# Optimization experiments

Measured on AMD Instinct MI355X. Metric: run time of the kernel, lower is better.

The kernel has to match this reference:

```python
import jax, jax.numpy as jnp
import numpy as np

B = 1
DIM = 128
NUM_HEADS = 8
HEAD_DIM = DIM // NUM_HEADS
RES = (4, 16, 16, 16)            # (L, D, H, W)
FINE = (2, 8, 8, 8)
COARSE = (1, 2, 2, 2)
FINE_STRIDE = tuple(r // f for r, f in zip(RES, FINE))      # (2,2,2,2)
COARSE_STRIDE = tuple(r // c for r, c in zip(RES, COARSE))  # (4,8,8,8)
LOCAL = (1, 2, 2, 2)
HIDDEN = 512
SCALE = HEAD_DIM ** -0.5
EPS = 1e-5
_DN = jax.lax.ConvDimensionNumbers((0, 1, 2, 3, 4, 5), (0, 1, 2, 3, 4, 5), (0, 1, 2, 3, 4, 5))


def conv4d(x, w, b, stride=(1, 1, 1, 1)):
    # x: (B, L, C, D, H, W); channel axis is 2 (matches repo Conv4d usage). 'same'-style k//2 pad.
    xc = jnp.transpose(x, (0, 2, 1, 3, 4, 5))  # B,C,L,D,H,W
    pads = [(k // 2, k // 2) for k in w.shape[2:]]
    y = jax.lax.conv_general_dilated(xc, w, window_strides=stride, padding=pads, dimension_numbers=_DN)
    y = y + b[None, :, None, None, None, None]
    return jnp.transpose(y, (0, 2, 1, 3, 4, 5))


def layernorm(x, w, b):
    mu = jnp.mean(x, -1, keepdims=True)
    var = jnp.mean(jnp.square(x - mu), -1, keepdims=True)
    return (x - mu) * jax.lax.rsqrt(var + EPS) * w + b


def cnorm(x, w, b):
    # LayerNorm over channel axis (axis 2) of (B,L,C,D,H,W)
    xt = jnp.transpose(x, (0, 1, 3, 4, 5, 2))
    xt = layernorm(xt, w, b)
    return jnp.transpose(xt, (0, 1, 5, 2, 3, 4))


def to_tokens(t):
    # (B,L,C,D,H,W) -> (B, L*D*H*W, C)
    b, c = t.shape[0], t.shape[2]
    return jnp.swapaxes(jnp.transpose(t, (0, 2, 1, 3, 4, 5)).reshape(b, c, -1), 1, 2)


def split_heads(t):
    b, n, c = t.shape
    return jnp.transpose(t.reshape(b, n, NUM_HEADS, c // NUM_HEADS), (0, 2, 1, 3))


def slg(x, q_w, q_b, k_w, k_b, v_w, v_b, p_w, p_b, f_w, f_b, c_w, c_b, ln_w, ln_b):
    Bx, L, C, D, H, W = x.shape
    N = L * D * H * W
    q = split_heads(to_tokens(conv4d(x, q_w, q_b)))          # (B,h,N,hd)
    xc = conv4d(x, c_w, c_b, COARSE_STRIDE)                  # coarse pyramid (B,1,C,2,2,2)
    xf = conv4d(x, f_w, f_b, FINE_STRIDE)                    # fine pyramid   (B,2,C,8,8,8)
    kc = to_tokens(conv4d(xc, k_w, k_b))
    kf = to_tokens(conv4d(xf, k_w, k_b))
    vc = to_tokens(conv4d(xc, v_w, v_b))
    vf = to_tokens(conv4d(xf, v_w, v_b))
    k = split_heads(layernorm(jnp.concatenate([kc, kf], 1), ln_w, ln_b))
    v = split_heads(layernorm(jnp.concatenate([vc, vf], 1), ln_w, ln_b))
    attn = jax.nn.softmax(jnp.einsum('bhqd,bhkd->bhqk', q, k) * SCALE, axis=-1)
    y = jnp.einsum('bhqk,bhkd->bhqd', attn, v)               # (B,h,N,hd)
    y = jnp.transpose(y, (0, 2, 1, 3)).reshape(Bx, N, C)
    y = jnp.swapaxes(jnp.swapaxes(y, 1, 2).reshape(Bx, C, L, D, H, W), 1, 2)
    return conv4d(y, p_w, p_b)


def _win(t):
    # (B,Lh,C,D,H,W) -> (B, n_windows, heads, win_tokens, hd)
    b, l, c, d, h, w = t.shape
    ll, ld, lh, lw = LOCAL
    nl, nd, nh, nw = l // ll, d // ld, h // lh, w // lw
    t = jnp.transpose(t, (0, 2, 1, 3, 4, 5)).reshape(b, c, nl, ll, nd, ld, nh, lh, nw, lw)
    t = jnp.transpose(t, (0, 2, 4, 6, 8, 3, 5, 7, 9, 1))
    t = t.reshape(b, nl * nd * nh * nw, ll * ld * lh * lw, NUM_HEADS, c // NUM_HEADS)
    return jnp.transpose(t, (0, 1, 3, 2, 4))


def _unwin(y, shape):
    b, l, c, d, h, w = shape
    ll, ld, lh, lw = LOCAL
    nl, nd, nh, nw = l // ll, d // ld, h // lh, w // lw
    y = jnp.transpose(y, (0, 1, 3, 2, 4)).reshape(b, nl, nd, nh, nw, ll, ld, lh, lw, c)
    y = jnp.transpose(y, (0, 9, 1, 5, 2, 6, 3, 7, 4, 8)).reshape(b, c, l, d, h, w)
    return jnp.swapaxes(y, 1, 2)


def tlg(x, q_w, q_b, k_w, k_b, v_w, v_b, p_w, p_b):
    # stage < 2: first temporal half cross-attends with second half (windowed)
    L = x.shape[1]
    xs, xe = x[:, :L // 2], x[:, L // 2:]

    def cross(xq, xkv):
        q = _win(conv4d(xq, q_w, q_b))
        k = _win(conv4d(xkv, k_w, k_b))
        v = _win(conv4d(xkv, v_w, v_b))
        a = jax.nn.softmax(jnp.einsum('bnhqd,bnhkd->bnhqk', q, k) * SCALE, axis=-1)
        y = _unwin(jnp.einsum('bnhqk,bnhkd->bnhqd', a, v), xq.shape)
        return conv4d(y, p_w, p_b)

    return jnp.concatenate([cross(xs, xe), cross(xe, xs)], axis=1)


def _forward(x, n1_w, n1_b, tq_w, tq_b, tk_w, tk_b, tv_w, tv_b, tp_w, tp_b,
             n2_w, n2_b, sq_w, sq_b, sk_w, sk_b, sv_w, sv_b, sp_w, sp_b,
             sf_w, sf_b, sc_w, sc_b, sn_w, sn_b,
             n3_w, n3_b, m1_w, m1_b, m2_w, m2_b):
    x = x + tlg(cnorm(x, n1_w, n1_b), tq_w, tq_b, tk_w, tk_b, tv_w, tv_b, tp_w, tp_b)
    x = x + slg(cnorm(x, n2_w, n2_b), sq_w, sq_b, sk_w, sk_b, sv_w, sv_b, sp_w, sp_b,
                sf_w, sf_b, sc_w, sc_b, sn_w, sn_b)
    x = x + conv4d(jax.nn.relu(conv4d(cnorm(x, n3_w, n3_b), m1_w, m1_b)), m2_w, m2_b)
    return x


def setup_inputs():
    keys = iter(jax.random.split(jax.random.key(0), 64))

    def rn(shape, s=0.02):
        return jax.random.normal(next(keys), shape, dtype=jnp.float32) * s

    L, D, H, W = RES
    inp = {"x": jax.random.normal(next(keys), (B, L, DIM, D, H, W), dtype=jnp.float32)}
    for n in ("n1", "n2", "n3", "sn"):
        inp[n + "_w"] = jnp.ones((DIM,), jnp.float32)
        inp[n + "_b"] = jnp.zeros((DIM,), jnp.float32)
    for n in ("tq", "tk", "tv", "tp"):
        inp[n + "_w"] = rn((DIM, DIM, 3, 1, 1, 1))
        inp[n + "_b"] = jnp.zeros((DIM,), jnp.float32)
    for n in ("sq", "sk", "sv", "sp", "sf", "sc"):
        inp[n + "_w"] = rn((DIM, DIM, 1, 3, 3, 3))
        inp[n + "_b"] = jnp.zeros((DIM,), jnp.float32)
    inp["m1_w"] = rn((HIDDEN, DIM, 3, 3, 3, 3))
    inp["m1_b"] = jnp.zeros((HIDDEN,), jnp.float32)
    inp["m2_w"] = rn((DIM, HIDDEN, 3, 3, 3, 3))
    inp["m2_b"] = jnp.zeros((DIM,), jnp.float32)
    return inp


def reference(x, n1_w, n1_b, n2_w, n2_b, n3_w, n3_b, sn_w, sn_b,
              tq_w, tq_b, tk_w, tk_b, tv_w, tv_b, tp_w, tp_b,
              sq_w, sq_b, sk_w, sk_b, sv_w, sv_b, sp_w, sp_b,
              sf_w, sf_b, sc_w, sc_b, m1_w, m1_b, m2_w, m2_b):
    return _forward(x, n1_w, n1_b, tq_w, tq_b, tk_w, tk_b, tv_w, tv_b, tp_w, tp_b,
                    n2_w, n2_b, sq_w, sq_b, sk_w, sk_b, sv_w, sv_b, sp_w, sp_b,
                    sf_w, sf_b, sc_w, sc_b, sn_w, sn_b,
                    n3_w, n3_b, m1_w, m1_b, m2_w, m2_b)
```

## Files before the change

### kernel.cpp

```cpp
#include <hip/hip_runtime.h>

typedef unsigned short u16;
typedef __attribute__((ext_vector_type(8))) short bf16x8;
typedef __attribute__((ext_vector_type(4))) float f32x4;

#define PITCH 40

__device__ __forceinline__ u16 f2bf(float f) {
  union { float f; unsigned u; } v; v.f = f;
  unsigned r = v.u + 0x7fffu + ((v.u >> 16) & 1u);
  return (u16)(r >> 16);
}
__device__ __forceinline__ float bf2f(u16 h) {
  union { unsigned u; float f; } v; v.u = ((unsigned)h) << 16;
  return v.f;
}
__device__ __forceinline__ float4 load4bf(const u16* p) {
  ushort4 h = *(const ushort4*)p;
  return make_float4(bf2f(h.x), bf2f(h.y), bf2f(h.z), bf2f(h.w));
}
__device__ __forceinline__ void gll16(const u16* g, u16* l) {
  __builtin_amdgcn_global_load_lds(
      (const __attribute__((address_space(1))) unsigned int*)g,
      (__attribute__((address_space(3))) unsigned int*)l, 16, 0, 0);
}

__device__ __forceinline__ ushort2 ln_row(float2 v, float2 gv, float2 bv) {
  float s = v.x + v.y;
#pragma unroll
  for (int o = 32; o > 0; o >>= 1) s += __shfl_xor(s, o);
  float mu = s * (1.0f / 128.0f);
  float dx = v.x - mu, dy = v.y - mu;
  float q = dx * dx + dy * dy;
#pragma unroll
  for (int o = 32; o > 0; o >>= 1) q += __shfl_xor(q, o);
  float rs = rsqrtf(q * (1.0f / 128.0f) + 1e-5f);
  ushort2 o2;
  o2.x = f2bf(dx * rs * gv.x + bv.x);
  o2.y = f2bf(dy * rs * gv.y + bv.y);
  return o2;
}

__global__ __launch_bounds__(256) void k_tin_ln(const float* __restrict__ x,
                                                float* __restrict__ X0,
                                                const float* __restrict__ g,
                                                const float* __restrict__ b,
                                                u16* __restrict__ XN) {
  __shared__ float t[128][33];
  int s0 = blockIdx.x * 32, l = blockIdx.y;
  int tid = threadIdx.x;
#pragma unroll
  for (int r = 0; r < 4; ++r) {
    int lin = r * 256 + tid;
    int c = lin >> 3, sq = (lin & 7) * 4;
    float4 v = *(const float4*)(x + ((long)(l * 128 + c) << 12) + s0 + sq);
    t[c][sq] = v.x; t[c][sq + 1] = v.y; t[c][sq + 2] = v.z; t[c][sq + 3] = v.w;
  }
  __syncthreads();
  int wave = tid >> 6, lane = tid & 63;
  int c2 = lane * 2;
  float2 gv = *(const float2*)(g + c2);
  float2 bv = *(const float2*)(b + c2);
#pragma unroll
  for (int p = 0; p < 8; ++p) {
    int s = p * 4 + wave;
    float2 v = make_float2(t[c2][s], t[c2 + 1][s]);
    long token = (long)l * 4096 + s0 + s;
    *(float2*)(X0 + token * 128 + c2) = v;
    ushort2 o2 = ln_row(v, gv, bv);
    *(ushort2*)(XN + token * 128 + c2) = o2;
  }
}

struct RAargs { const float* w[12]; u16* wb[12]; u16* zp; };
__global__ __launch_bounds__(256) void k_repack_all(RAargs a) {
  __shared__ float ws[128 * 81];
  int z = blockIdx.z, x = blockIdx.x, tid = threadIdx.x;
  if (z == 0 && x == 0) ((unsigned long long*)a.zp)[tid] = 0ull;
  if (z < 10 && x >= 128) return;
  int NT = (z < 4) ? 3 : ((z < 10) ? 27 : 81);
  int OC = (z == 10) ? 512 : 128;
  int IC = (z == 11) ? 512 : 128;
  int oc, ic0;
  if (z == 11) { oc = x & 127; ic0 = (x >> 7) << 7; }
  else { oc = x; ic0 = 0; }
  const float* src = a.w[z] + ((long)oc * IC + ic0) * NT;
  int n = 128 * NT;
  for (int i = tid; i < n; i += 256) ws[i] = src[i];
  __syncthreads();
  u16* dst = a.wb[z] + (long)oc * IC + ic0;
  long tstep = (long)OC * IC;
  for (int idx = tid; idx < n; idx += 256) {
    int t = idx >> 7, i = idx & 127;
    dst[(long)t * tstep + i] = f2bf(ws[i * NT + t]);
  }
}

struct QC {
  const u16* X[4]; const u16* W[4]; const float* B[4]; void* Y[4];
  int M[4];
  int lgo[4][3];
  int lgi[4][3];
  int di[4][3];
  int st[4][4];
  int flags[4];
};
__global__ __launch_bounds__(256) void k_conv_quad(QC a) {
  __shared__ u16 As[64 * PITCH];
  __shared__ u16 Bs[64 * PITCH];
  int grp = blockIdx.z;
  int M = a.M[grp];
  int m0 = blockIdx.x * 64;
  if (m0 >= M) return;
  const u16* X = a.X[grp];
  const u16* W3 = a.W[grp];
  const float* bias = a.B[grp];
  void* Yv = a.Y[grp];
  int lgWo = a.lgo[grp][0], lgHo = a.lgo[grp][1], lgDo = a.lgo[grp][2];
  int lgWi = a.lgi[grp][0], lgHi = a.lgi[grp][1], lgDi = a.lgi[grp][2];
  int Di = a.di[grp][0], Hi = a.di[grp][1], Wi = a.di[grp][2];
  int sL = a.st[grp][0], sD = a.st[grp][1], sH = a.st[grp][2], sW = a.st[grp][3];
  int flags = a.flags[grp];

  int tid = threadIdx.x;
  int wave = tid >> 6, lane = tid & 63;
  int quad = lane >> 4, l15 = lane & 15;
  int oc0 = blockIdx.y * 64;

  int srl = tid >> 2;
  int sao = (tid & 3) * 8;
  int sboc = tid >> 2, sbo = (tid & 3) * 8;

  int sm = m0 + srl;
  bool mv = sm < M;
  int w = sm & ((1 << lgWo) - 1);
  int h = (sm >> lgWo) & ((1 << lgHo) - 1);
  int d = (sm >> (lgWo + lgHo)) & ((1 << lgDo) - 1);
  int l = sm >> (lgWo + lgHo + lgDo);

  int c0 = 0, c1 = 0, c2 = 0, c3 = 0;
  auto comp_nb = [&]() -> long {
    if (!mv) return -1;
    int li = l * sL, di = d * sD + c2 - 1, hi = h * sH + c1 - 1, wi = w * sW + c0 - 1;
    bool ok = ((unsigned)di < (unsigned)Di) && ((unsigned)hi < (unsigned)Hi) &&
              ((unsigned)wi < (unsigned)Wi);
    (void)c3;
    if (!ok) return -1;
    return ((((long)((li << lgDi) + di) << lgHi) + hi) << lgWi) + wi;
  };

  long nb = comp_nb();
  const u16* wt = W3 + (long)(oc0 + sboc) * 128 + sbo;
  const long wstep = 128 * 128;
  const int kmask = 3;
  const int total = 27 * 4;

  const bf16x8 Z = {0, 0, 0, 0, 0, 0, 0, 0};
  bf16x8 ra0 = Z, rb;
  if (nb >= 0) ra0 = *(const bf16x8*)(X + nb * 128 + sao);
  rb = *(const bf16x8*)wt;

  f32x4 acc[4];
#pragma unroll
  for (int j = 0; j < 4; ++j) acc[j] = {0.f, 0.f, 0.f, 0.f};

  int wrow = wave * 16;

  for (int ks = 0; ks < total; ++ks) {
    __syncthreads();
    *(bf16x8*)&As[srl * PITCH + sao] = ra0;
    *(bf16x8*)&Bs[sboc * PITCH + sbo] = rb;
    __syncthreads();
    int ksn = ks + 1;
    if (ksn < total) {
      int k0n = (ksn & kmask) << 5;
      if ((ksn & kmask) == 0) {
        wt += wstep;
        if (++c0 == 3) { c0 = 0; if (++c1 == 3) { c1 = 0; if (++c2 == 3) { c2 = 0; ++c3; } } }
        nb = comp_nb();
      }
      ra0 = Z;
      if (nb >= 0) ra0 = *(const bf16x8*)(X + nb * 128 + k0n + sao);
      rb = *(const bf16x8*)(wt + k0n);
    }
    bf16x8 a0 = *(const bf16x8*)&As[(wrow + l15) * PITCH + quad * 8];
#pragma unroll
    for (int j = 0; j < 4; ++j) {
      bf16x8 b = *(const bf16x8*)&Bs[(j * 16 + l15) * PITCH + quad * 8];
      acc[j] = __builtin_amdgcn_mfma_f32_16x16x32_bf16(a0, b, acc[j], 0, 0, 0);
    }
  }

  int col = oc0 + l15;
#pragma unroll
  for (int j = 0; j < 4; ++j) {
    float bj = bias[col + j * 16];
    int rbase = m0 + wrow + quad * 4;
#pragma unroll
    for (int r = 0; r < 4; ++r) {
      int row = rbase + r;
      if (row >= M) continue;
      float v = acc[j][r] + bj;
      if (flags & 2) v = fmaxf(v, 0.f);
      long off = (long)row * 128 + col + j * 16;
      if (flags & 4) ((u16*)Yv)[off] = f2bf(v);
      else if (flags & 1) ((float*)Yv)[off] += v;
      else ((float*)Yv)[off] = v;
    }
  }
}

__global__ __launch_bounds__(256, 4) void k_conv_gl(
    const u16* __restrict__ X, const u16* __restrict__ W3,
    const float* __restrict__ bias, void* __restrict__ Yv, float* __restrict__ SP,
    const u16* __restrict__ ZP,
    int M, int IC, int OC, int mode, int NT, int NSPLIT, long wgs,
    int lgWo, int lgHo, int lgDo,
    int lgWi, int lgHi, int lgDi,
    int Li, int Di, int Hi, int Wi,
    int sL, int sD, int sH, int sW, int flags) {
  __shared__ __align__(16) u16 As[128 * 64];
  __shared__ __align__(16) u16 Bs[128 * 64];
  int tid = threadIdx.x;
  int wave = tid >> 6, lane = tid & 63;
  int quad = lane >> 4, l15 = lane & 15;
  int m0 = blockIdx.x * 128, oc0 = blockIdx.y * 128;
  int mi = wave & 1, ni = wave >> 1;
  int zz = blockIdx.z;
  int grp = zz / NSPLIT, split = zz % NSPLIT;
  W3 += (long)grp * wgs;

  int rp[4], cA[4], sm[4];
#pragma unroll
  for (int q = 0; q < 4; ++q) {
    rp[q] = wave * 32 + q * 8 + (lane >> 3);
    cA[q] = ((lane & 7) - (rp[q] >> 1)) & 7;
    sm[q] = m0 + rp[q];
  }

  int tap_per = (NT + NSPLIT - 1) / NSPLIT;
  int t0 = split * tap_per;
  int t1 = min(NT, t0 + tap_per);
  int kc = IC >> 6;
  int total = (t1 - t0) * kc;

  int c0 = t0 % 3, c1 = (t0 / 3) % 3, c2 = (t0 / 9) % 3, c3 = t0 / 27;
  auto comp_nb = [&](int smv) -> int {
    if (smv >= M) return -1;
    int w = smv & ((1 << lgWo) - 1);
    int h = (smv >> lgWo) & ((1 << lgHo) - 1);
    int d = (smv >> (lgWo + lgHo)) & ((1 << lgDo) - 1);
    int l = smv >> (lgWo + lgHo + lgDo);
    int li, di, hi, wi; bool ok;
    if (mode == 0) {
      int dl = c0 - 1;
      int ll = (l & 1) + dl;
      ok = (ll >= 0 && ll < 2);
      li = l + dl; di = d; hi = h; wi = w;
    } else if (mode == 1) {
      li = l * sL; di = d * sD + c2 - 1; hi = h * sH + c1 - 1; wi = w * sW + c0 - 1;
      ok = ((unsigned)di < (unsigned)Di) && ((unsigned)hi < (unsigned)Hi) &&
           ((unsigned)wi < (unsigned)Wi);
    } else {
      li = l + c3 - 1; di = d + c2 - 1; hi = h + c1 - 1; wi = w + c0 - 1;
      ok = ((unsigned)li < (unsigned)Li) && ((unsigned)di < (unsigned)Di) &&
           ((unsigned)hi < (unsigned)Hi) && ((unsigned)wi < (unsigned)Wi);
    }
    if (!ok) return -1;
    return (((li << lgDi) + di) << lgHi | hi) << lgWi | wi;
  };

  int nb[4];
#pragma unroll
  for (int q = 0; q < 4; ++q) nb[q] = comp_nb(sm[q]);
  long wstep = (long)OC * IC;
  const u16* wbase = W3 + (long)t0 * wstep + (long)oc0 * IC;

  f32x4 acc[4][4];
#pragma unroll
  for (int i = 0; i < 4; ++i)
#pragma unroll
    for (int j = 0; j < 4; ++j) acc[i][j] = {0.f, 0.f, 0.f, 0.f};

  int kk = 0;
  for (int ks = 0; ks < total; ++ks) {
    if (kk == kc) {
      kk = 0;
      if (++c0 == 3) { c0 = 0; if (++c1 == 3) { c1 = 0; if (++c2 == 3) { c2 = 0; ++c3; } } }
#pragma unroll
      for (int q = 0; q < 4; ++q) nb[q] = comp_nb(sm[q]);
      wbase += wstep;
    }
    int k0 = kk << 6;
    ++kk;
    __syncthreads();
#pragma unroll
    for (int q = 0; q < 4; ++q) {
      const u16* a = (nb[q] >= 0) ? X + (long)nb[q] * IC + k0 + cA[q] * 8 : ZP;
      gll16(a, &As[(wave * 4 + q) * 512]);
    }
#pragma unroll
    for (int q = 0; q < 4; ++q) {
      const u16* bsrc = wbase + (long)rp[q] * IC + k0 + cA[q] * 8;
      gll16(bsrc, &Bs[(wave * 4 + q) * 512]);
    }
    __syncthreads();
#pragma unroll
    for (int ksub = 0; ksub < 2; ++ksub) {
      bf16x8 af[4], bf[4];
#pragma unroll
      for (int i = 0; i < 4; ++i) {
        int row = mi * 64 + i * 16 + l15;
        int pa = ((ksub * 4 + quad) + (row >> 1)) & 7;
        af[i] = *(const bf16x8*)&As[row * 64 + pa * 8];
      }
#pragma unroll
      for (int j = 0; j < 4; ++j) {
        int row = ni * 64 + j * 16 + l15;
        int pb = ((ksub * 4 + quad) + (row >> 1)) & 7;
        bf[j] = *(const bf16x8*)&Bs[row * 64 + pb * 8];
      }
#pragma unroll
      for (int i = 0; i < 4; ++i)
#pragma unroll
        for (int j = 0; j < 4; ++j)
          acc[i][j] = __builtin_amdgcn_mfma_f32_16x16x32_bf16(af[i], bf[j], acc[i][j], 0, 0, 0);
    }
  }

  if (NSPLIT > 1) {
    float* out = SP + (long)(grp * NSPLIT + split) * M * OC;
#pragma unroll
    for (int j = 0; j < 4; ++j) {
      int c = oc0 + ni * 64 + j * 16 + l15;
#pragma unroll
      for (int i = 0; i < 4; ++i) {
        int rbase = m0 + mi * 64 + i * 16 + quad * 4;
#pragma unroll
        for (int r = 0; r < 4; ++r) {
          int row = rbase + r;
          if (row < M) out[(long)row * OC + c] = acc[i][j][r];
        }
      }
    }
  } else {
#pragma unroll
    for (int j = 0; j < 4; ++j) {
      int c = oc0 + ni * 64 + j * 16 + l15;
      float bj = bias[c];
#pragma unroll
      for (int i = 0; i < 4; ++i) {
        int rbase = m0 + mi * 64 + i * 16 + quad * 4;
#pragma unroll
        for (int r = 0; r < 4; ++r) {
          int row = rbase + r;
          if (row >= M) continue;
          float v = acc[i][j][r] + bj;
          if (flags & 2) v = fmaxf(v, 0.f);
          long off = (long)row * OC + c;
          if (flags & 4) ((u16*)Yv)[off] = f2bf(v);
          else if (flags & 1) ((float*)Yv)[off] += v;
          else ((float*)Yv)[off] = v;
        }
      }
    }
  }
}

__global__ __launch_bounds__(512, 2) void k_conv_g256(
    const u16* __restrict__ X, const u16* __restrict__ W3,
    const float* __restrict__ bias, void* __restrict__ Yv, float* __restrict__ SP,
    const u16* __restrict__ ZP,
    int M, int IC, int OC, int mode, int NT, int NSPLIT,
    int lgWo, int lgHo, int lgDo,
    int lgWi, int lgHi, int lgDi,
    int Li, int Di, int Hi, int Wi,
    int sL, int sD, int sH, int sW, int flags) {
  __shared__ __align__(16) u16 Ab[4][8192];
  __shared__ __align__(16) u16 Bb[4][8192];
  int tid = threadIdx.x;
  int wave = tid >> 6, lane = tid & 63;
  int quad = lane >> 4, l15 = lane & 15;
  int wr = wave >> 2, wc = wave & 3;
  int m0 = blockIdx.x * 256, oc0 = blockIdx.y * 256;

  int srow0 = tid >> 2;
  int spc = tid & 3;
  int lc0 = (spc - (srow0 >> 1)) & 3;
  int lc1 = (spc - ((srow0 + 128) >> 1)) & 3;

  int kc = IC >> 6;
  int hsPerTap = kc << 1;
  int tap_per = (NT + NSPLIT - 1) / NSPLIT;
  int t0 = blockIdx.z * tap_per;
  int t1 = min(NT, t0 + tap_per);
  int TOT = (t1 - t0) * kc;
  int TOTH = TOT * 2;

  int c0 = t0 % 3, c1 = (t0 / 3) % 3, c2 = (t0 / 9) % 3, c3 = t0 / 27;
  auto comp_nb = [&](int smv) -> int {
    if (smv >= M) return -1;
    int w = smv & ((1 << lgWo) - 1);
    int h = (smv >> lgWo) & ((1 << lgHo) - 1);
    int d = (smv >> (lgWo + lgHo)) & ((1 << lgDo) - 1);
    int l = smv >> (lgWo + lgHo + lgDo);
    int li, di, hi, wi; bool ok;
    if (mode == 0) {
      int dl = c0 - 1;
      int ll = (l & 1) + dl;
      ok = (ll >= 0 && ll < 2);
      li = l + dl; di = d; hi = h; wi = w;
    } else if (mode == 1) {
      li = l * sL; di = d * sD + c2 - 1; hi = h * sH + c1 - 1; wi = w * sW + c0 - 1;
      ok = ((unsigned)di < (unsigned)Di) && ((unsigned)hi < (unsigned)Hi) &&
           ((unsigned)wi < (unsigned)Wi);
    } else {
      li = l + c3 - 1; di = d + c2 - 1; hi = h + c1 - 1; wi = w + c0 - 1;
      ok = ((unsigned)li < (unsigned)Li) && ((unsigned)di < (unsigned)Di) &&
// ... 126 lines not shown
  }

  if (NSPLIT > 1) {
    float* outp = SP + (long)blockIdx.z * M * OC;
#pragma unroll
    for (int i = 0; i < 8; ++i)
#pragma unroll
      for (int j = 0; j < 4; ++j) {
        int c = oc0 + (wc << 6) + (j << 4) + l15;
        int rb = m0 + (wr << 7) + (i << 4) + (quad << 2);
#pragma unroll
        for (int r = 0; r < 4; ++r) {
          int row = rb + r;
          if (row < M) outp[(long)row * OC + c] = acc[i][j][r];
        }
      }
  } else {
#pragma unroll
    for (int i = 0; i < 8; ++i)
#pragma unroll
      for (int j = 0; j < 4; ++j) {
        int c = oc0 + (wc << 6) + (j << 4) + l15;
        float bj = bias[c];
        int rb = m0 + (wr << 7) + (i << 4) + (quad << 2);
#pragma unroll
        for (int r = 0; r < 4; ++r) {
          int row = rb + r;
          if (row >= M) continue;
          float v = acc[i][j][r] + bj;
          if (flags & 2) v = fmaxf(v, 0.f);
          long off = (long)row * OC + c;
          if (flags & 4) ((u16*)Yv)[off] = f2bf(v);
          else if (flags & 1) ((float*)Yv)[off] += v;
          else ((float*)Yv)[off] = v;
        }
      }
  }
}

__global__ __launch_bounds__(256) void k_combine(const float* __restrict__ SP,
                                                 const float* __restrict__ bias,
                                                 void* __restrict__ out,
                                                 long MOC, int lgOC, int nsplit, int flags) {
  long idx = (long)blockIdx.x * 256 + threadIdx.x;
  if (idx >= MOC) return;
  float v = bias[idx & ((1 << lgOC) - 1)];
  for (int s = 0; s < nsplit; ++s) v += SP[s * MOC + idx];
  if (flags & 2) v = fmaxf(v, 0.f);
  if (flags & 4) ((u16*)out)[idx] = f2bf(v);
  else if (flags & 1) ((float*)out)[idx] += v;
  else ((float*)out)[idx] = v;
}

__global__ __launch_bounds__(256) void k_combine3(const float* __restrict__ SP,
                                                  const float* __restrict__ b0,
                                                  const float* __restrict__ b1,
                                                  const float* __restrict__ b2,
                                                  u16* __restrict__ out,
                                                  int lgMOC, int lgOC, int nsplit, int ngrp) {
  long idx = (long)blockIdx.x * 256 + threadIdx.x;
  long tot = (long)ngrp << lgMOC;
  if (idx >= tot) return;
  int grp = (int)(idx >> lgMOC);
  long sub = idx & ((1L << lgMOC) - 1);
  const float* bp = (grp == 0) ? b0 : ((grp == 1) ? b1 : b2);
  float v = bp[sub & ((1 << lgOC) - 1)];
  const float* sp = SP + (((long)grp * nsplit) << lgMOC);
  for (int s = 0; s < nsplit; ++s) v += sp[((long)s << lgMOC) + sub];
  out[idx] = f2bf(v);
}

__global__ __launch_bounds__(256) void k_comb_ln(const float* __restrict__ SP,
                                                 const float* __restrict__ bias,
                                                 float* __restrict__ X0,
                                                 const float* __restrict__ g,
                                                 const float* __restrict__ b,
                                                 u16* __restrict__ XN, int nsplit) {
  int n = blockIdx.x * 4 + (threadIdx.x >> 6);
  int lane = threadIdx.x & 63;
  long off = (long)n * 128 + lane * 2;
  float2 v = *(const float2*)(bias + lane * 2);
  for (int s = 0; s < nsplit; ++s) {
    float2 sv = *(const float2*)(SP + (((long)s) << 21) + off);
    v.x += sv.x; v.y += sv.y;
  }
  float2 x0 = *(const float2*)(X0 + off);
  v.x += x0.x; v.y += x0.y;
  *(float2*)(X0 + off) = v;
  float2 gv = *(const float2*)(g + lane * 2);
  float2 bv = *(const float2*)(b + lane * 2);
  ushort2 o2 = ln_row(v, gv, bv);
  *(ushort2*)(XN + off) = o2;
}

__global__ __launch_bounds__(256) void k_comb_out(const float* __restrict__ SP,
                                                  const float* __restrict__ X0,
                                                  const float* __restrict__ bias,
                                                  float* __restrict__ out) {
  __shared__ float t[32][33];
  int s0 = blockIdx.x * 32, c0 = blockIdx.y * 32, l = blockIdx.z;
  int r = threadIdx.x >> 3, q4 = (threadIdx.x & 7) * 4;
  long token = (long)l * 4096 + s0 + r;
  long off = token * 128 + c0 + q4;
  float4 v = *(const float4*)(bias + c0 + q4);
#pragma unroll
  for (int s = 0; s < 8; ++s) {
    float4 sv = *(const float4*)(SP + (((long)s) << 21) + off);
    v.x += sv.x; v.y += sv.y; v.z += sv.z; v.w += sv.w;
  }
  float4 x0 = *(const float4*)(X0 + off);
  v.x += x0.x; v.y += x0.y; v.z += x0.z; v.w += x0.w;
  t[r][q4] = v.x; t[r][q4 + 1] = v.y; t[r][q4 + 2] = v.z; t[r][q4 + 3] = v.w;
  __syncthreads();
  float4 o = {t[q4][r], t[q4 + 1][r], t[q4 + 2][r], t[q4 + 3][r]};
  *(float4*)(out + ((long)(l * 128 + c0 + r) << 12) + s0 + q4) = o;
}

__global__ __launch_bounds__(256) void k_tlg_attn(const u16* __restrict__ Q,
                                                  const u16* __restrict__ K,
                                                  const u16* __restrict__ V,
                                                  u16* __restrict__ Y) {
  int gw = blockIdx.x * 4 + (threadIdx.x >> 6);
  int lane = threadIdx.x & 63;
  int head = gw & 7;
  int win = gw >> 3;
  int wB = win & 7, hB = (win >> 3) & 7, dB = (win >> 6) & 7, l = win >> 9;
  int i = lane >> 3, j = lane & 7;
  int nq = (l << 12) | ((dB * 2 + (i >> 2)) << 8) | ((hB * 2 + ((i >> 1) & 1)) << 4) |
           (wB * 2 + (i & 1));
  int lk = l ^ 2;
  int nk = (lk << 12) | ((dB * 2 + (j >> 2)) << 8) | ((hB * 2 + ((j >> 1) & 1)) << 4) |
           (wB * 2 + (j & 1));
  int hoff = head * 16;
  const u16* qp = Q + (long)nq * 128 + hoff;
  const u16* kp = K + (long)nk * 128 + hoff;
  float s = 0.f;
#pragma unroll
  for (int t = 0; t < 16; t += 4) {
    float4 a = load4bf(qp + t);
    float4 b = load4bf(kp + t);
    s += a.x * b.x + a.y * b.y + a.z * b.z + a.w * b.w;
  }
  s *= 0.25f;
  float mx = s;
#pragma unroll
  for (int o = 1; o < 8; o <<= 1) mx = fmaxf(mx, __shfl_xor(mx, o));
  float e = __expf(s - mx);
  float sum = e;
#pragma unroll
  for (int o = 1; o < 8; o <<= 1) sum += __shfl_xor(sum, o);
  float p = e / sum;
  const u16* vp = V + (long)nk * 128 + hoff;
  float y[16];
#pragma unroll
  for (int t = 0; t < 16; t += 4) {
    float4 vv = load4bf(vp + t);
    y[t] = p * vv.x; y[t + 1] = p * vv.y; y[t + 2] = p * vv.z; y[t + 3] = p * vv.w;
  }
#pragma unroll
  for (int o = 1; o < 8; o <<= 1) {
#pragma unroll
    for (int t = 0; t < 16; ++t) y[t] += __shfl_xor(y[t], o);
  }
  if (j == 0) {
    u16* yp = Y + (long)nq * 128 + hoff;
    u16 tmp[16];
#pragma unroll
    for (int t = 0; t < 16; ++t) tmp[t] = f2bf(y[t]);
    *(uint4*)(yp) = *(uint4*)tmp;
    *(uint4*)(yp + 8) = *(uint4*)(tmp + 8);
  }
}

__global__ __launch_bounds__(256) void k_ln_kv(const float* __restrict__ X,
                                               const float* __restrict__ g,
                                               const float* __restrict__ b,
                                               u16* __restrict__ Kh,
                                               u16* __restrict__ Vt) {
  int n = blockIdx.x * 4 + (threadIdx.x >> 6);
  if (n >= 2064) return;
  int lane = threadIdx.x & 63;
  float2 v = *(const float2*)(X + (long)n * 128 + lane * 2);
  float2 gv = *(const float2*)(g + lane * 2);
  float2 bv = *(const float2*)(b + lane * 2);
  ushort2 o2 = ln_row(v, gv, bv);
  int isK = n < 1032;
  int k = isK ? n : n - 1032;
  int h = lane >> 3, d = (lane & 7) * 2;
  if (isK) {
    *(ushort2*)(Kh + (((long)h * 1032 + k) << 4) + d) = o2;
  } else {
    Vt[((long)(h * 16 + d)) * 1032 + k] = o2.x;
    Vt[((long)(h * 16 + d) + 1) * 1032 + k] = o2.y;
  }
}

__global__ __launch_bounds__(256) void k_slg_flash(const u16* __restrict__ Q,
                                                   const u16* __restrict__ Kh,
                                                   const u16* __restrict__ Vt,
                                                   u16* __restrict__ Y) {
  constexpr int NK = 1032;
  constexpr int NTILE = 17;
  __shared__ __align__(16) u16 Ks[64 * 24];
  __shared__ __align__(16) u16 Vs[16 * 72];
  __shared__ __align__(16) u16 Ps[4][16 * 72];
  int tid = threadIdx.x;
  int wave = tid >> 6, lane = tid & 63;
  int quad = lane >> 4, l15 = lane & 15;
  int h = blockIdx.x & 7;
  int q0 = (blockIdx.x >> 3) * 64 + wave * 16;

  const bf16x8 Zb = {0, 0, 0, 0, 0, 0, 0, 0};
  bf16x8 qf = Zb;
  if (quad < 2) qf = *(const bf16x8*)(Q + (long)(q0 + l15) * 128 + h * 16 + quad * 8);

  const u16* Kbase = Kh + (long)h * NK * 16;
  const u16* Vbase = Vt + (long)h * 16 * NK;

  float mrow[4], lrow[4];
  f32x4 oacc = {0.f, 0.f, 0.f, 0.f};
#pragma unroll
  for (int r = 0; r < 4; ++r) { mrow[r] = -1e30f; lrow[r] = 0.f; }

  int skey = tid >> 2, sch = (tid & 3) * 4;
  int svd = tid >> 4, svc = (tid & 15) * 4;

  for (int t = 0; t < NTILE; ++t) {
    int k0 = t * 64;
    __syncthreads();
    {
      short4 v = {0, 0, 0, 0};
      int key = k0 + skey;
      if (key < NK) v = *(const short4*)(Kbase + key * 16 + sch);
      *(short4*)&Ks[skey * 24 + sch] = v;
    }
    {
      short4 v = {0, 0, 0, 0};
      int colb = k0 + svc;
      if (colb < NK) v = *(const short4*)(Vbase + svd * NK + colb);
      *(short4*)&Vs[svd * 72 + svc] = v;
    }
    __syncthreads();

    f32x4 s[4];
#pragma unroll
    for (int sub = 0; sub < 4; ++sub) {
      bf16x8 b = Zb;
      if (quad < 2) b = *(const bf16x8*)&Ks[(sub * 16 + l15) * 24 + quad * 8];
      f32x4 zero = {0.f, 0.f, 0.f, 0.f};
      s[sub] = __builtin_amdgcn_mfma_f32_16x16x32_bf16(qf, b, zero, 0, 0, 0);
    }
    float pv[4][4];
    float tmax[4] = {-1e30f, -1e30f, -1e30f, -1e30f};
#pragma unroll
    for (int sub = 0; sub < 4; ++sub) {
      int key = k0 + sub * 16 + l15;
      bool valid = key < NK;
#pragma unroll
      for (int r = 0; r < 4; ++r) {
        float sv = valid ? s[sub][r] * 0.25f : -1e30f;
        pv[sub][r] = sv;
        tmax[r] = fmaxf(tmax[r], sv);
      }
    }
#pragma unroll
    for (int o = 1; o < 16; o <<= 1)
#pragma unroll
// ... 37 lines not shown
    Y[(long)(q0 + quad * 4 + r) * 128 + h * 16 + l15] = f2bf(oacc[r] * inv);
  }
}

static inline int ilg(int v) { int r = 0; while ((1 << r) < v) ++r; return r; }

extern "C" void kernel_launch(void* const* d_in, const int* in_sizes, int n_in,
                              void* d_out, int out_size, void* d_ws, size_t ws_size,
                              hipStream_t stream) {
  (void)in_sizes; (void)n_in; (void)out_size; (void)ws_size;
  const float* x    = (const float*)d_in[0];
  const float* n1_w = (const float*)d_in[1];  const float* n1_b = (const float*)d_in[2];
  const float* n2_w = (const float*)d_in[3];  const float* n2_b = (const float*)d_in[4];
  const float* n3_w = (const float*)d_in[5];  const float* n3_b = (const float*)d_in[6];
  const float* sn_w = (const float*)d_in[7];  const float* sn_b = (const float*)d_in[8];
  const float* tq_w = (const float*)d_in[9];  const float* tq_b = (const float*)d_in[10];
  const float* tk_w = (const float*)d_in[11]; const float* tk_b = (const float*)d_in[12];
  const float* tv_w = (const float*)d_in[13]; const float* tv_b = (const float*)d_in[14];
  const float* tp_w = (const float*)d_in[15]; const float* tp_b = (const float*)d_in[16];
  const float* sq_w = (const float*)d_in[17]; const float* sq_b = (const float*)d_in[18];
  const float* sk_w = (const float*)d_in[19]; const float* sk_b = (const float*)d_in[20];
  const float* sv_w = (const float*)d_in[21]; const float* sv_b = (const float*)d_in[22];
  const float* sp_w = (const float*)d_in[23]; const float* sp_b = (const float*)d_in[24];
  const float* sf_w = (const float*)d_in[25]; const float* sf_b = (const float*)d_in[26];
  const float* sc_w = (const float*)d_in[27]; const float* sc_b = (const float*)d_in[28];
  const float* m1_w = (const float*)d_in[29]; const float* m1_b = (const float*)d_in[30];
  const float* m2_w = (const float*)d_in[31]; const float* m2_b = (const float*)d_in[32];

  char* p = (char*)d_ws;
  auto alloc = [&](size_t bytes) { char* r = p; p += (bytes + 255) & ~(size_t)255; return r; };
  const long N = 16384;
  float* X0 = (float*)alloc(N * 128 * 4);
  u16* XN = (u16*)alloc(N * 128 * 2);
  u16* Qb = (u16*)alloc(N * 128 * 2);
  u16* Kb = (u16*)alloc(N * 128 * 2);
  u16* Vb = (u16*)alloc(N * 128 * 2);
  u16* Yb = (u16*)alloc(N * 128 * 2);
  u16* H  = (u16*)alloc(N * 512 * 2);
  u16* XC = (u16*)alloc(8 * 128 * 2);
  u16* XF = (u16*)alloc(1024 * 128 * 2);
  float* Kf = (float*)alloc(1032 * 128 * 4);
  float* Vf = (float*)alloc(1032 * 128 * 4);
  u16* Kh = (u16*)alloc(8 * 1032 * 16 * 2);
  u16* Vt = (u16*)alloc(8 * 16 * 1032 * 2);
  float* SPb = (float*)alloc(2L * N * 512 * 4);
  u16* ZPb = (u16*)alloc(2048);
  u16* tq2 = (u16*)alloc(49152 * 2);  u16* tk2 = (u16*)alloc(49152 * 2);
  u16* tv2 = (u16*)alloc(49152 * 2);  u16* tp2 = (u16*)alloc(49152 * 2);
  u16* sq2 = (u16*)alloc(442368 * 2); u16* sk2 = (u16*)alloc(442368 * 2);
  u16* sv2 = (u16*)alloc(442368 * 2); u16* sp2 = (u16*)alloc(442368 * 2);
  u16* sf2 = (u16*)alloc(442368 * 2); u16* sc2 = (u16*)alloc(442368 * 2);
  u16* m12 = (u16*)alloc(5308416L * 2);
  u16* m22 = (u16*)alloc(5308416L * 2);

  {
    RAargs ra;
    const float* ws[12] = {tq_w, tk_w, tv_w, tp_w, sq_w, sk_w, sv_w, sp_w, sf_w, sc_w,
                           m1_w, m2_w};
    u16* wbs[12] = {tq2, tk2, tv2, tp2, sq2, sk2, sv2, sp2, sf2, sc2, m12, m22};
    for (int i = 0; i < 12; ++i) { ra.w[i] = ws[i]; ra.wb[i] = wbs[i]; }
    ra.zp = ZPb;
    k_repack_all<<<dim3(512, 1, 12), 256, 0, stream>>>(ra);
  }

  auto conv_gl = [&](const u16* Xp, const u16* Wp, const float* Bp, void* Yp,
                     int M, int IC, int OC, int mode, int NT, int nsplit, int flags) {
    dim3 g(M / 128, OC / 128, nsplit);
    k_conv_gl<<<g, 256, 0, stream>>>(Xp, Wp, Bp, Yp, SPb, ZPb, M, IC, OC, mode, NT, nsplit,
                                     0L, 4, 4, 4, 4, 4, 4, 4, 16, 16, 16, 1, 1, 1, 1, flags);
    if (nsplit > 1 && flags >= 0) {
      long MOC = (long)M * OC;
      k_combine<<<(int)((MOC + 255) / 256), 256, 0, stream>>>(SPb, Bp, Yp, MOC, ilg(OC),
                                                              nsplit, flags);
    }
  };
  auto conv_gl256 = [&](const u16* Xp, const u16* Wp, const float* Bp, void* Yp,
                        int M, int IC, int OC, int mode, int NT, int nsplit, int flags) {
    dim3 g(M / 256, OC / 256, nsplit);
    k_conv_g256<<<g, 512, 0, stream>>>(Xp, Wp, Bp, Yp, SPb, ZPb, M, IC, OC, mode, NT, nsplit,
                                       4, 4, 4, 4, 4, 4, 4, 16, 16, 16, 1, 1, 1, 1, flags);
    if (nsplit > 1) {
      long MOC = (long)M * OC;
      k_combine<<<(int)((MOC + 255) / 256), 256, 0, stream>>>(SPb, Bp, Yp, MOC, ilg(OC),
                                                              nsplit, flags);
    }
  };

  k_tin_ln<<<dim3(128, 4), 256, 0, stream>>>(x, X0, n1_w, n1_b, XN);

  {
    dim3 g(128, 1, 6);
    k_conv_gl<<<g, 256, 0, stream>>>(XN, tq2, tq_b, Qb, SPb, ZPb, 16384, 128, 128, 0, 3, 2,
                                     49152L, 4, 4, 4, 4, 4, 4, 4, 16, 16, 16, 1, 1, 1, 1, 4);
    k_combine3<<<24576, 256, 0, stream>>>(SPb, tq_b, tk_b, tv_b, Qb, 21, 7, 2, 3);
  }
  k_tlg_attn<<<4096, 256, 0, stream>>>(Qb, Kb, Vb, Yb);
  {
    dim3 g(128, 1, 3);
    k_conv_gl<<<g, 256, 0, stream>>>(Yb, tp2, tp_b, X0, SPb, ZPb, 16384, 128, 128, 0, 3, 3,
                                     0L, 4, 4, 4, 4, 4, 4, 4, 16, 16, 16, 1, 1, 1, 1, 1);
    k_comb_ln<<<4096, 256, 0, stream>>>(SPb, tp_b, X0, n2_w, n2_b, XN, 3);
  }

  conv_gl(XN, sq2, sq_b, Qb, 16384, 128, 128, 1, 27, 7, 4);
  {
    QC q{};
    q.X[0] = XN; q.W[0] = sc2; q.B[0] = sc_b; q.Y[0] = XC; q.M[0] = 8;
    q.lgo[0][0] = 1; q.lgo[0][1] = 1; q.lgo[0][2] = 1;
    q.lgi[0][0] = 4; q.lgi[0][1] = 4; q.lgi[0][2] = 4;
    q.di[0][0] = 16; q.di[0][1] = 16; q.di[0][2] = 16;
    q.st[0][0] = 4; q.st[0][1] = 8; q.st[0][2] = 8; q.st[0][3] = 8;
    q.flags[0] = 4;
    q.X[1] = XN; q.W[1] = sf2; q.B[1] = sf_b; q.Y[1] = XF; q.M[1] = 1024;
    q.lgo[1][0] = 3; q.lgo[1][1] = 3; q.lgo[1][2] = 3;
    q.lgi[1][0] = 4; q.lgi[1][1] = 4; q.lgi[1][2] = 4;
    q.di[1][0] = 16; q.di[1][1] = 16; q.di[1][2] = 16;
    q.st[1][0] = 2; q.st[1][1] = 2; q.st[1][2] = 2; q.st[1][3] = 2;
    q.flags[1] = 4;
    k_conv_quad<<<dim3(16, 2, 2), 256, 0, stream>>>(q);
  }
  {
    QC q{};
    for (int i = 0; i < 4; ++i) {
      int fine = i >> 1, isv = i & 1;
      q.X[i] = fine ? XF : XC;
      q.W[i] = isv ? sv2 : sk2;
      q.B[i] = isv ? sv_b : sk_b;
      q.Y[i] = (void*)((isv ? Vf : Kf) + (fine ? 8 * 128 : 0));
      q.M[i] = fine ? 1024 : 8;
      int lo = fine ? 3 : 1;
      q.lgo[i][0] = lo; q.lgo[i][1] = lo; q.lgo[i][2] = lo;
      int li = fine ? 3 : 1;
      q.lgi[i][0] = li; q.lgi[i][1] = li; q.lgi[i][2] = li;
      int dd = fine ? 8 : 2;
      q.di[i][0] = dd; q.di[i][1] = dd; q.di[i][2] = dd;
      q.st[i][0] = 1; q.st[i][1] = 1; q.st[i][2] = 1; q.st[i][3] = 1;
      q.flags[i] = 0;
    }
    k_conv_quad<<<dim3(16, 2, 4), 256, 0, stream>>>(q);
  }
  k_ln_kv<<<516, 256, 0, stream>>>(Kf, sn_w, sn_b, Kh, Vt);
  k_slg_flash<<<2048, 256, 0, stream>>>(Qb, Kh, Vt, Yb);
  {
    dim3 g(128, 1, 7);
    k_conv_gl<<<g, 256, 0, stream>>>(Yb, sp2, sp_b, X0, SPb, ZPb, 16384, 128, 128, 1, 27, 7,
                                     0L, 4, 4, 4, 4, 4, 4, 4, 16, 16, 16, 1, 1, 1, 1, 1);
    k_comb_ln<<<4096, 256, 0, stream>>>(SPb, sp_b, X0, n3_w, n3_b, XN, 7);
  }

  conv_gl256(XN, m12, m1_b, H, 16384, 128, 512, 2, 81, 2, 6);
  {
    dim3 g(128, 1, 8);
    k_conv_gl<<<g, 256, 0, stream>>>(H, m22, m2_b, X0, SPb, ZPb, 16384, 512, 128, 2, 81, 8,
                                     0L, 4, 4, 4, 4, 4, 4, 4, 16, 16, 16, 1, 1, 1, 1, 1);
    k_comb_out<<<dim3(128, 4, 4), 256, 0, stream>>>(SPb, X0, m2_b, (float*)d_out);
  }
}
```

Before: 877.7 us.

## Fuse split-K combines into consumers and merge small kernels into shared launches

The input transpose+LayerNorm moves into the weight-repack launch as an extra grid slice. The QKV combine kernel is removed: temporal attention now sums the split-K partials and biases itself. The sq conv runs in the same launch as the coarse/fine pyramid convs, and the spatial flash kernel sums the seven sq partials inline when it loads Q. This cuts launches and a full write/read pass of Q/K/V in bf16, at the cost of the attention kernels reading fp32 partials redundantly (K/V partials are re-read by several query waves).

Result: faster. 852.9 us (-2.8%).

```diff
diff --git a/kernel.cpp b/kernel.cpp
--- a/kernel.cpp
+++ b/kernel.cpp
@@ -41,41 +41,39 @@
   return o2;
 }
 
-__global__ __launch_bounds__(256) void k_tin_ln(const float* __restrict__ x,
-                                                float* __restrict__ X0,
-                                                const float* __restrict__ g,
-                                                const float* __restrict__ b,
-                                                u16* __restrict__ XN) {
-  __shared__ float t[128][33];
-  int s0 = blockIdx.x * 32, l = blockIdx.y;
-  int tid = threadIdx.x;
-#pragma unroll
-  for (int r = 0; r < 4; ++r) {
-    int lin = r * 256 + tid;
-    int c = lin >> 3, sq = (lin & 7) * 4;
-    float4 v = *(const float4*)(x + ((long)(l * 128 + c) << 12) + s0 + sq);
-    t[c][sq] = v.x; t[c][sq + 1] = v.y; t[c][sq + 2] = v.z; t[c][sq + 3] = v.w;
-  }
-  __syncthreads();
-  int wave = tid >> 6, lane = tid & 63;
-  int c2 = lane * 2;
-  float2 gv = *(const float2*)(g + c2);
-  float2 bv = *(const float2*)(b + c2);
-#pragma unroll
-  for (int p = 0; p < 8; ++p) {
-    int s = p * 4 + wave;
-    float2 v = make_float2(t[c2][s], t[c2 + 1][s]);
-    long token = (long)l * 4096 + s0 + s;
-    *(float2*)(X0 + token * 128 + c2) = v;
-    ushort2 o2 = ln_row(v, gv, bv);
-    *(ushort2*)(XN + token * 128 + c2) = o2;
-  }
-}
-
-struct RAargs { const float* w[12]; u16* wb[12]; u16* zp; };
+struct RAargs {
+  const float* w[12]; u16* wb[12]; u16* zp;
+  const float* x; float* X0; const float* g; const float* b; u16* XN;
+};
 __global__ __launch_bounds__(256) void k_repack_all(RAargs a) {
-  __shared__ float ws[128 * 81];
+  __shared__ __align__(16) float ws[128 * 81];
   int z = blockIdx.z, x = blockIdx.x, tid = threadIdx.x;
+  if (z == 12) {
+    float (*t)[33] = (float (*)[33])ws;
+    int s0 = (x & 127) * 32, l = x >> 7;
+#pragma unroll
+    for (int r = 0; r < 4; ++r) {
+      int lin = r * 256 + tid;
+      int c = lin >> 3, sq = (lin & 7) * 4;
+      float4 v = *(const float4*)(a.x + ((long)(l * 128 + c) << 12) + s0 + sq);
+      t[c][sq] = v.x; t[c][sq + 1] = v.y; t[c][sq + 2] = v.z; t[c][sq + 3] = v.w;
+    }
+    __syncthreads();
+    int wave = tid >> 6, lane = tid & 63;
+    int c2 = lane * 2;
+    float2 gv = *(const float2*)(a.g + c2);
+    float2 bv = *(const float2*)(a.b + c2);
+#pragma unroll
+    for (int pq = 0; pq < 8; ++pq) {
+      int s = pq * 4 + wave;
+      float2 v = make_float2(t[c2][s], t[c2 + 1][s]);
+      long token = (long)l * 4096 + s0 + s;
+      *(float2*)(a.X0 + token * 128 + c2) = v;
+      ushort2 o2 = ln_row(v, gv, bv);
+      *(ushort2*)(a.XN + token * 128 + c2) = o2;
+    }
+    return;
+  }
   if (z == 0 && x == 0) ((unsigned long long*)a.zp)[tid] = 0ull;
   if (z < 10 && x >= 128) return;
   int NT = (z < 4) ? 3 : ((z < 10) ? 27 : 81);
@@ -105,10 +103,7 @@
   int st[4][4];
   int flags[4];
 };
-__global__ __launch_bounds__(256) void k_conv_quad(QC a) {
-  __shared__ u16 As[64 * PITCH];
-  __shared__ u16 Bs[64 * PITCH];
-  int grp = blockIdx.z;
+__device__ __forceinline__ void conv_quad_body(u16* As, u16* Bs, const QC& a, int grp) {
   int M = a.M[grp];
   int m0 = blockIdx.x * 64;
   if (m0 >= M) return;
@@ -210,25 +205,27 @@
   }
 }
 
-__global__ __launch_bounds__(256, 4) void k_conv_gl(
+__global__ __launch_bounds__(256) void k_conv_quad(QC a) {
+  __shared__ u16 As[64 * PITCH];
+  __shared__ u16 Bs[64 * PITCH];
+  conv_quad_body(As, Bs, a, blockIdx.z);
+}
+
+__device__ __forceinline__ void conv_gl_body(
+    u16* As, u16* Bs,
     const u16* __restrict__ X, const u16* __restrict__ W3,
-    const float* __restrict__ bias, void* __restrict__ Yv, float* __restrict__ SP,
-    const u16* __restrict__ ZP,
-    int M, int IC, int OC, int mode, int NT, int NSPLIT, long wgs,
+    const float* __restrict__ bias, void* __restrict__ Yv,
+    float* __restrict__ SP, const u16* __restrict__ ZP,
+    int M, int IC, int OC, int mode, int NT, int NSPLIT, int split, int spidx,
     int lgWo, int lgHo, int lgDo,
     int lgWi, int lgHi, int lgDi,
     int Li, int Di, int Hi, int Wi,
     int sL, int sD, int sH, int sW, int flags) {
-  __shared__ __align__(16) u16 As[128 * 64];
-  __shared__ __align__(16) u16 Bs[128 * 64];
   int tid = threadIdx.x;
   int wave = tid >> 6, lane = tid & 63;
   int quad = lane >> 4, l15 = lane & 15;
   int m0 = blockIdx.x * 128, oc0 = blockIdx.y * 128;
   int mi = wave & 1, ni = wave >> 1;
-  int zz = blockIdx.z;
-  int grp = zz / NSPLIT, split = zz % NSPLIT;
-  W3 += (long)grp * wgs;
 
   int rp[4], cA[4], sm[4];
 #pragma unroll
@@ -329,7 +326,7 @@
   }
 
   if (NSPLIT > 1) {
-    float* out = SP + (long)(grp * NSPLIT + split) * M * OC;
+    float* out = SP + (long)spidx * M * OC;
 #pragma unroll
     for (int j = 0; j < 4; ++j) {
       int c = oc0 + ni * 64 + j * 16 + l15;
@@ -364,6 +361,42 @@
         }
       }
     }
+  }
+}
+
+__global__ __launch_bounds__(256, 4) void k_conv_gl(
+    const u16* __restrict__ X, const u16* __restrict__ W3,
+    const float* __restrict__ bias, void* __restrict__ Yv, float* __restrict__ SP,
+    const u16* __restrict__ ZP,
+    int M, int IC, int OC, int mode, int NT, int NSPLIT, long wgs,
+    int lgWo, int lgHo, int lgDo,
+    int lgWi, int lgHi, int lgDi,
+    int Li, int Di, int Hi, int Wi,
+    int sL, int sD, int sH, int sW, int flags) {
+  __shared__ __align__(16) u16 As[128 * 64];
+  __shared__ __align__(16) u16 Bs[128 * 64];
+  int zz = blockIdx.z;
+  int grp = zz / NSPLIT, split = zz % NSPLIT;
+  conv_gl_body(As, Bs, X, W3 + (long)grp * wgs, bias, Yv, SP, ZP,
+               M, IC, OC, mode, NT, NSPLIT, split, zz,
+               lgWo, lgHo, lgDo, lgWi, lgHi, lgDi,
+               Li, Di, Hi, Wi, sL, sD, sH, sW, flags);
+}
+
+__global__ __launch_bounds__(256, 4) void k_sq_scsf(
+    const u16* __restrict__ XN, const u16* __restrict__ W3,
+    float* __restrict__ SP, const u16* __restrict__ ZP, QC qa) {
+  __shared__ __align__(16) u16 As[128 * 64];
+  __shared__ __align__(16) u16 Bs[128 * 64];
+  int z = blockIdx.z;
+  if (z < 7) {
+    if (blockIdx.y) return;
+    conv_gl_body(As, Bs, XN, W3, nullptr, nullptr, SP, ZP,
+                 16384, 128, 128, 1, 27, 7, z, z,
+                 4, 4, 4, 4, 4, 4, 4, 16, 16, 16, 1, 1, 1, 1, 0);
+  } else {
+    if (blockIdx.x >= 16) return;
+    conv_quad_body(As, Bs, qa, z - 7);
   }
 }
 
@@ -596,24 +629,6 @@
   else ((float*)out)[idx] = v;
 }
 
-__global__ __launch_bounds__(256) void k_combine3(const float* __restrict__ SP,
-                                                  const float* __restrict__ b0,
-                                                  const float* __restrict__ b1,
-                                                  const float* __restrict__ b2,
-                                                  u16* __restrict__ out,
-                                                  int lgMOC, int lgOC, int nsplit, int ngrp) {
-  long idx = (long)blockIdx.x * 256 + threadIdx.x;
-  long tot = (long)ngrp << lgMOC;
-  if (idx >= tot) return;
-  int grp = (int)(idx >> lgMOC);
-  long sub = idx & ((1L << lgMOC) - 1);
-  const float* bp = (grp == 0) ? b0 : ((grp == 1) ? b1 : b2);
-  float v = bp[sub & ((1 << lgOC) - 1)];
-  const float* sp = SP + (((long)grp * nsplit) << lgMOC);
-  for (int s = 0; s < nsplit; ++s) v += sp[((long)s << lgMOC) + sub];
-  out[idx] = f2bf(v);
-}
-
 __global__ __launch_bounds__(256) void k_comb_ln(const float* __restrict__ SP,
                                                  const float* __restrict__ bias,
                                                  float* __restrict__ X0,
@@ -660,9 +675,10 @@
   *(float4*)(out + ((long)(l * 128 + c0 + r) << 12) + s0 + q4) = o;
 }
 
-__global__ __launch_bounds__(256) void k_tlg_attn(const u16* __restrict__ Q,
-                                                  const u16* __restrict__ K,
-                                                  const u16* __restrict__ V,
+__global__ __launch_bounds__(256) void k_tlg_attn(const float* __restrict__ SP,
+                                                  const float* __restrict__ bq,
+                                                  const float* __restrict__ bk,
+                                                  const float* __restrict__ bv,
                                                   u16* __restrict__ Y) {
   int gw = blockIdx.x * 4 + (threadIdx.x >> 6);
   int lane = threadIdx.x & 63;
@@ -676,14 +692,27 @@
   int nk = (lk << 12) | ((dB * 2 + (j >> 2)) << 8) | ((hB * 2 + ((j >> 1) & 1)) << 4) |
            (wB * 2 + (j & 1));
   int hoff = head * 16;
-  const u16* qp = Q + (long)nq * 128 + hoff;
-  const u16* kp = K + (long)nk * 128 + hoff;
+  long qoff = (long)nq * 128 + hoff;
+  long koff = (long)nk * 128 + hoff;
+  const float* S1 = SP + (1L << 21);
+  const float* S2 = SP + (2L << 21);
+  const float* S3 = SP + (3L << 21);
+  const float* S4 = SP + (4L << 21);
+  const float* S5 = SP + (5L << 21);
   float s = 0.f;
 #pragma unroll
   for (int t = 0; t < 16; t += 4) {
-    float4 a = load4bf(qp + t);
-    float4 b = load4bf(kp + t);
-    s += a.x * b.x + a.y * b.y + a.z * b.z + a.w * b.w;
+    float4 a0 = *(const float4*)(SP + qoff + t);
+    float4 a1 = *(const float4*)(S1 + qoff + t);
+    float4 ab = *(const float4*)(bq + hoff + t);
+    float4 b0 = *(const float4*)(S2 + koff + t);
+    float4 b1 = *(const float4*)(S3 + koff + t);
+    float4 bb = *(const float4*)(bk + hoff + t);
+    float ax = a0.x + a1.x + ab.x, ay = a0.y + a1.y + ab.y;
+    float az = a0.z + a1.z + ab.z, aw = a0.w + a1.w + ab.w;
+    float bx = b0.x + b1.x + bb.x, by = b0.y + b1.y + bb.y;
+    float bz = b0.z + b1.z + bb.z, bw = b0.w + b1.w + bb.w;
+    s += ax * bx + ay * by + az * bz + aw * bw;
   }
   s *= 0.25f;
   float mx = s;
@@ -694,12 +723,16 @@
 #pragma unroll
   for (int o = 1; o < 8; o <<= 1) sum += __shfl_xor(sum, o);
   float p = e / sum;
-  const u16* vp = V + (long)nk * 128 + hoff;
   float y[16];
 #pragma unroll
   for (int t = 0; t < 16; t += 4) {
-    float4 vv = load4bf(vp + t);
-    y[t] = p * vv.x; y[t + 1] = p * vv.y; y[t + 2] = p * vv.z; y[t + 3] = p * vv.w;
+    float4 v0 = *(const float4*)(S4 + koff + t);
+    float4 v1 = *(const float4*)(S5 + koff + t);
+    float4 vb = *(const float4*)(bv + hoff + t);
+    y[t] = p * (v0.x + v1.x + vb.x);
+    y[t + 1] = p * (v0.y + v1.y + vb.y);
+    y[t + 2] = p * (v0.z + v1.z + vb.z);
+    y[t + 3] = p * (v0.w + v1.w + vb.w);
   }
 #pragma unroll
   for (int o = 1; o < 8; o <<= 1) {
@@ -739,7 +772,8 @@
   }
 }
 
-__global__ __launch_bounds__(256) void k_slg_flash(const u16* __restrict__ Q,
+__global__ __launch_bounds__(256) void k_slg_flash(const float* __restrict__ QSP,
+                                                   const float* __restrict__ bq,
                                                    const u16* __restrict__ Kh,
                                                    const u16* __restrict__ Vt,
                                                    u16* __restrict__ Y) {
@@ -756,7 +790,23 @@
 
   const bf16x8 Zb = {0, 0, 0, 0, 0, 0, 0, 0};
   bf16x8 qf = Zb;
-  if (quad < 2) qf = *(const bf16x8*)(Q + (long)(q0 + l15) * 128 + h * 16 + quad * 8);
+  if (quad < 2) {
+    long off = (long)(q0 + l15) * 128 + h * 16 + quad * 8;
+    float v[8];
+#pragma unroll
+    for (int jj = 0; jj < 8; ++jj) v[jj] = bq[h * 16 + quad * 8 + jj];
+#pragma unroll
+    for (int sx = 0; sx < 7; ++sx) {
+      float4 p0 = *(const float4*)(QSP + ((long)sx << 21) + off);
+      float4 p1 = *(const float4*)(QSP + ((long)sx << 21) + off + 4);
+      v[0] += p0.x; v[1] += p0.y; v[2] += p0.z; v[3] += p0.w;
+      v[4] += p1.x; v[5] += p1.y; v[6] += p1.z; v[7] += p1.w;
+    }
+    union { u16 u[8]; bf16x8 v8; } cv;
+#pragma unroll
+    for (int jj = 0; jj < 8; ++jj) cv.u[jj] = f2bf(v[jj]);
+    qf = cv.v8;
+  }
 
   const u16* Kbase = Kh + (long)h * NK * 16;
   const u16* Vbase = Vt + (long)h * 16 * NK;
@@ -900,6 +950,7 @@
   u16* sf2 = (u16*)alloc(442368 * 2); u16* sc2 = (u16*)alloc(442368 * 2);
   u16* m12 = (u16*)alloc(5308416L * 2);
   u16* m22 = (u16*)alloc(5308416L * 2);
+  (void)Kb; (void)Vb;
 
   {
     RAargs ra;
@@ -907,8 +958,8 @@
                            m1_w, m2_w};
     u16* wbs[12] = {tq2, tk2, tv2, tp2, sq2, sk2, sv2, sp2, sf2, sc2, m12, m22};
     for (int i = 0; i < 12; ++i) { ra.w[i] = ws[i]; ra.wb[i] = wbs[i]; }
-    ra.zp = ZPb;
-    k_repack_all<<<dim3(512, 1, 12), 256, 0, stream>>>(ra);
+    ra.zp = ZPb; ra.x = x; ra.X0 = X0; ra.g = n1_w; ra.b = n1_b; ra.XN = XN;
+    k_repack_all<<<dim3(512, 1, 13), 256, 0, stream>>>(ra);
   }
 
   auto conv_gl = [&](const u16* Xp, const u16* Wp, const float* Bp, void* Yp,
@@ -916,41 +967,17 @@
     dim3 g(M / 128, OC / 128, nsplit);
     k_conv_gl<<<g, 256, 0, stream>>>(Xp, Wp, Bp, Yp, SPb, ZPb, M, IC, OC, mode, NT, nsplit,
                                      0L, 4, 4, 4, 4, 4, 4, 4, 16, 16, 16, 1, 1, 1, 1, flags);
-    if (nsplit > 1 && flags >= 0) {
-      long MOC = (long)M * OC;
-      k_combine<<<(int)((MOC + 255) / 256), 256, 0, stream>>>(SPb, Bp, Yp, MOC, ilg(OC),
-                                                              nsplit, flags);
-    }
   };
-  auto conv_gl256 = [&](const u16* Xp, const u16* Wp, const float* Bp, void* Yp,
-                        int M, int IC, int OC, int mode, int NT, int nsplit, int flags) {
-    dim3 g(M / 256, OC / 256, nsplit);
-    k_conv_g256<<<g, 512, 0, stream>>>(Xp, Wp, Bp, Yp, SPb, ZPb, M, IC, OC, mode, NT, nsplit,
-                                       4, 4, 4, 4, 4, 4, 4, 16, 16, 16, 1, 1, 1, 1, flags);
-    if (nsplit > 1) {
-      long MOC = (long)M * OC;
-      k_combine<<<(int)((MOC + 255) / 256), 256, 0, stream>>>(SPb, Bp, Yp, MOC, ilg(OC),
-                                                              nsplit, flags);
-    }
-  };
-
-  k_tin_ln<<<dim3(128, 4), 256, 0, stream>>>(x, X0, n1_w, n1_b, XN);
 
   {
     dim3 g(128, 1, 6);
     k_conv_gl<<<g, 256, 0, stream>>>(XN, tq2, tq_b, Qb, SPb, ZPb, 16384, 128, 128, 0, 3, 2,
                                      49152L, 4, 4, 4, 4, 4, 4, 4, 16, 16, 16, 1, 1, 1, 1, 4);
-    k_combine3<<<24576, 256, 0, stream>>>(SPb, tq_b, tk_b, tv_b, Qb, 21, 7, 2, 3);
-  }
-  k_tlg_attn<<<4096, 256, 0, stream>>>(Qb, Kb, Vb, Yb);
-  {
-    dim3 g(128, 1, 3);
-    k_conv_gl<<<g, 256, 0, stream>>>(Yb, tp2, tp_b, X0, SPb, ZPb, 16384, 128, 128, 0, 3, 3,
-                                     0L, 4, 4, 4, 4, 4, 4, 4, 16, 16, 16, 1, 1, 1, 1, 1);
-    k_comb_ln<<<4096, 256, 0, stream>>>(SPb, tp_b, X0, n2_w, n2_b, XN, 3);
-  }
-
-  conv_gl(XN, sq2, sq_b, Qb, 16384, 128, 128, 1, 27, 7, 4);
+  }
+  k_tlg_attn<<<4096, 256, 0, stream>>>(SPb, tq_b, tk_b, tv_b, Yb);
+  conv_gl(Yb, tp2, tp_b, X0, 16384, 128, 128, 0, 3, 3, 1);
+  k_comb_ln<<<4096, 256, 0, stream>>>(SPb, tp_b, X0, n2_w, n2_b, XN, 3);
+
   {
     QC q{};
     q.X[0] = XN; q.W[0] = sc2; q.B[0] = sc_b; q.Y[0] = XC; q.M[0] = 8;
@@ -965,7 +992,7 @@
     q.di[1][0] = 16; q.di[1][1] = 16; q.di[1][2] = 16;
     q.st[1][0] = 2; q.st[1][1] = 2; q.st[1][2] = 2; q.st[1][3] = 2;
     q.flags[1] = 4;
-    k_conv_quad<<<dim3(16, 2, 2), 256, 0, stream>>>(q);
+    k_sq_scsf<<<dim3(128, 2, 9), 256, 0, stream>>>(XN, sq2, SPb, ZPb, q);
   }
   {
     QC q{};
@@ -988,19 +1015,17 @@
     k_conv_quad<<<dim3(16, 2, 4), 256, 0, stream>>>(q);
   }
   k_ln_kv<<<516, 256, 0, stream>>>(Kf, sn_w, sn_b, Kh, Vt);
-  k_slg_flash<<<2048, 256, 0, stream>>>(Qb, Kh, Vt, Yb);
+  k_slg_flash<<<2048, 256, 0, stream>>>(SPb, sq_b, Kh, Vt, Yb);
+  conv_gl(Yb, sp2, sp_b, X0, 16384, 128, 128, 1, 27, 7, 1);
+  k_comb_ln<<<4096, 256, 0, stream>>>(SPb, sp_b, X0, n3_w, n3_b, XN, 7);
+
   {
-    dim3 g(128, 1, 7);
-    k_conv_gl<<<g, 256, 0, stream>>>(Yb, sp2, sp_b, X0, SPb, ZPb, 16384, 128, 128, 1, 27, 7,
-                                     0L, 4, 4, 4, 4, 4, 4, 4, 16, 16, 16, 1, 1, 1, 1, 1);
-    k_comb_ln<<<4096, 256, 0, stream>>>(SPb, sp_b, X0, n3_w, n3_b, XN, 7);
-  }
-
-  conv_gl256(XN, m12, m1_b, H, 16384, 128, 512, 2, 81, 2, 6);
-  {
-    dim3 g(128, 1, 8);
-    k_conv_gl<<<g, 256, 0, stream>>>(H, m22, m2_b, X0, SPb, ZPb, 16384, 512, 128, 2, 81, 8,
-                                     0L, 4, 4, 4, 4, 4, 4, 4, 16, 16, 16, 1, 1, 1, 1, 1);
-    k_comb_out<<<dim3(128, 4, 4), 256, 0, stream>>>(SPb, X0, m2_b, (float*)d_out);
-  }
-}
+    dim3 g(64, 2, 2);
+    k_conv_g256<<<g, 512, 0, stream>>>(XN, m12, m1_b, H, SPb, ZPb, 16384, 128, 512, 2, 81, 2,
+                                       4, 4, 4, 4, 4, 4, 4, 16, 16, 16, 1, 1, 1, 1, 6);
+    long MOC = (long)16384 * 512;
+    k_combine<<<(int)((MOC + 255) / 256), 256, 0, stream>>>(SPb, m1_b, H, MOC, ilg(512), 2, 6);
+  }
+  conv_gl(H, m22, m2_b, X0, 16384, 512, 128, 2, 81, 8, 1);
+  k_comb_out<<<dim3(128, 4, 4), 256, 0, stream>>>(SPb, X0, m2_b, (float*)d_out);
+}
```
